# Optimization experiments

Hardware: AMD Instinct MI355X
Metric: run time of the kernel (lower is better)

Reference implementation:

```python
import jax, jax.numpy as jnp
import numpy as np

EPS = 1e-12

def _l2norm(x):
    # F.normalize(p=2, dim=1) with eps clamp on the norm
    n = jnp.linalg.norm(x, axis=1, keepdims=True)
    return x / jnp.maximum(n, EPS)

def _xavier_uniform(key, shape, gain=1.414):
    fan_in, fan_out = shape[-1], shape[0]
    a = gain * np.sqrt(6.0 / (fan_in + fan_out))
    return jax.random.uniform(key, shape, jnp.float32, -a, a)

def setup_inputs() -> dict:
    NUM_ENT, NUM_REL, D, E, B = 100000, 500, 512, 150000, 4096
    key = jax.random.key(0)
    ks = jax.random.split(key, 12)
    heads = jax.random.randint(ks[0], (B, 1), 0, NUM_ENT)
    rels  = jax.random.randint(ks[1], (B, 1), 0, NUM_REL)
    tails = jax.random.randint(ks[2], (B, 1), 0, NUM_ENT)
    triples = jnp.concatenate([heads, rels, tails], axis=1)           # [B,3]
    node_list = jax.random.randint(ks[3], (2, E), 0, NUM_ENT)          # [2,E] (src,dst)
    edge_list = jax.random.randint(ks[4], (E,), 0, NUM_REL)            # [E] relation per edge
    return {
        "triples": triples,
        "node_list": node_list,
        "edge_list": edge_list,
        "ent_emb_init": jax.random.normal(ks[5], (NUM_ENT, D), jnp.float32),
        "rel_emb_init": jax.random.normal(ks[6], (NUM_REL, D), jnp.float32),
        "W_1": _xavier_uniform(ks[7], (D, D)),
        "W_a": _xavier_uniform(ks[8], (1, D)),
        "g_0": _xavier_uniform(ks[9], (1, D)),
        "W_E": _xavier_uniform(ks[10], (D, D)),
        "W_R": _xavier_uniform(ks[11], (D, D)),
    }

def reference(triples, node_list, edge_list, ent_emb_init, rel_emb_init,
              W_1, W_a, g_0, W_E, W_R):
    num_ent = ent_emb_init.shape[0]
    e0 = _l2norm(ent_emb_init)                      # normalized entity table [N,D]
    src, dst = node_list[0], node_list[1]
    h_i = e0[src]                                   # [E,D]
    h_j = e0[dst]                                   # [E,D]
    g_k = rel_emb_init[edge_list]                   # [E,D]

    # c_ijk = W_1 @ (h_j*g_k)^T  -> kept edge-major as [E,D]
    c = (h_j * g_k) @ W_1.T                         # [E,D]
    a = -jax.nn.leaky_relu((h_i * jnp.tanh(c)) @ W_a[0], 0.2)   # [E]
    c_base = (h_i * g_0) @ W_1.T                    # [E,D]
    a_base = -jax.nn.leaky_relu((h_i * jnp.tanh(c_base)) @ W_a[0], 0.2)  # [E]

    a_exp = jnp.exp(a)                              # [E]
    ab_exp = jnp.exp(a_base)                        # [E]

    # segment-softmax denominator: sum of edge exps per source node + baseline term
    a_exp_sum = jax.ops.segment_sum(a_exp[:, None], src, num_segments=num_ent)  # [N,1]
    # baseline exp depends only on src node -> duplicate scatter-set writes identical values
    ab_sorted = jnp.zeros_like(a_exp_sum).at[src].set(ab_exp[:, None])           # [N,1]
    denom = ab_sorted + a_exp_sum
    denom = jnp.where(denom == 0.0, EPS, denom)

    # weighted scatter-aggregate of messages (dropout omitted: eval-mode identity)
    ac = a_exp[:, None] * c                         # [E,D]
    ac_base = ab_exp[:, None] * c_base              # [E,D]
    a_new = jax.ops.segment_sum(ac, src, num_segments=num_ent)                   # [N,D]
    ab_new = jnp.zeros_like(a_new).at[src].set(ac_base)                          # [N,D]

    h_prime = jax.nn.elu((ab_new + a_new) / denom)  # [N,D]
    ent_new = _l2norm(e0 @ W_E + h_prime)           # [N,D]
    rel_new = rel_emb_init @ W_R                    # [R,D]

    head = ent_new[triples[:, 0]][:, None, :]       # [B,1,D]
    rel  = rel_new[triples[:, 1]][:, None, :]       # [B,1,D]
    tail = ent_new[triples[:, 2]][:, None, :]       # [B,1,D]
    return jnp.concatenate([head, rel, tail], axis=1)  # [B,3,D]
```

## Files before the change

kernel.cpp:

```cpp
#include <hip/hip_runtime.h>
#include <cmath>


#define DDIM 512
#define MAXM 65536
#define GBM 128
#define GBN 128

typedef __attribute__((ext_vector_type(8))) short short8;
typedef __attribute__((ext_vector_type(4))) short short4v;
typedef __attribute__((ext_vector_type(4))) float fv4;
typedef unsigned short u16;

__device__ __forceinline__ float elu1(float x) { return x > 0.f ? x : expm1f(x); }
__device__ __forceinline__ float sexp(float x) {
    float lr = x >= 0.f ? x : 0.2f * x;
    return expf(-lr);
}
__device__ __forceinline__ u16 f2bf(float x) {
    unsigned u = __float_as_uint(x);
    u += 0x7FFFu + ((u >> 16) & 1u);
    return (u16)(u >> 16);
}
__device__ __forceinline__ float bf2f(u16 h) {
    return __uint_as_float((unsigned)h << 16);
}
__device__ __forceinline__ void cvt8(const float* v, short8& h8, short8& l8) {
    #pragma unroll
    for (int i = 0; i < 8; i++) {
        u16 h = f2bf(v[i]);
        h8[i] = (short)h;
        l8[i] = (short)f2bf(v[i] - bf2f(h));
    }
}
__device__ __forceinline__ void gld16(const void* g, void* l) {
    __builtin_amdgcn_global_load_lds(
        (const __attribute__((address_space(1))) unsigned int*)g,
        (__attribute__((address_space(3))) unsigned int*)l,
        16, 0, 0);
}

__global__ __launch_bounds__(128)
void invnorm_sel_kernel(const float* __restrict__ emb, const int* __restrict__ slotNode,
                        const int* __restrict__ rowsL, const int* __restrict__ dstIdx,
                        const int* __restrict__ Mdev, int NS, float* __restrict__ invN)
{
    __shared__ float ws2[2];
    int total = NS + min(MAXM, *Mdev);
    int t = threadIdx.x;
    for (int q = blockIdx.x; q < total; q += gridDim.x) {
        int n = (q < NS) ? slotNode[q] : dstIdx[rowsL[q - NS]];
        float4 v = *(const float4*)(emb + (size_t)n * DDIM + t * 4);
        float s = v.x*v.x + v.y*v.y + v.z*v.z + v.w*v.w;
        #pragma unroll
        for (int off = 32; off > 0; off >>= 1) s += __shfl_down(s, off);
        if ((t & 63) == 0) ws2[t >> 6] = s;
        __syncthreads();
        if (t == 0) invN[n] = 1.f / fmaxf(sqrtf(ws2[0] + ws2[1]), 1e-12f);
        __syncthreads();
    }
}

__global__ __launch_bounds__(128)
void l2norm_kernel(float* __restrict__ data)
{
    int r = blockIdx.x, t = threadIdx.x;
    size_t o = (size_t)r * DDIM + t * 4;
    float4 v = *(const float4*)(data + o);
    float s = v.x*v.x + v.y*v.y + v.z*v.z + v.w*v.w;
    #pragma unroll
    for (int off = 32; off > 0; off >>= 1) s += __shfl_down(s, off);
    __shared__ float ws2[2];
    if ((t & 63) == 0) ws2[t >> 6] = s;
    __syncthreads();
    float inv = 1.f / fmaxf(sqrtf(ws2[0] + ws2[1]), 1e-12f);
    *(float4*)(data + o) = make_float4(v.x*inv, v.y*inv, v.z*inv, v.w*inv);
}

__global__ void hist_kernel(const int* __restrict__ src, int* __restrict__ cnt, int E)
{
    int e = blockIdx.x * 256 + threadIdx.x;
    if (e < E) atomicAdd(&cnt[src[e]], 1);
}

__global__ __launch_bounds__(1024)
void scan1_kernel(const int* __restrict__ in, int* __restrict__ out,
                  int* __restrict__ blockTot, int n)
{
    __shared__ int sh[1024];
    int t = threadIdx.x;
    int i = blockIdx.x * 1024 + t;
    int v = (i < n) ? in[i] : 0;
    sh[t] = v;
    __syncthreads();
    for (int off = 1; off < 1024; off <<= 1) {
        int x = (t >= off) ? sh[t - off] : 0;
        __syncthreads();
        sh[t] += x;
        __syncthreads();
    }
    if (i < n) out[i] = sh[t] - v;
    if (t == 1023) blockTot[blockIdx.x] = sh[1023];
}

__global__ __launch_bounds__(1024)
void scan2_kernel(const int* __restrict__ blockTot, int* __restrict__ blockOff,
                  int* __restrict__ outLast, int G)
{
    __shared__ int sh[1024];
    int t = threadIdx.x;
    int v = (t < G) ? blockTot[t] : 0;
    sh[t] = v;
    __syncthreads();
    for (int off = 1; off < 1024; off <<= 1) {
        int x = (t >= off) ? sh[t - off] : 0;
        __syncthreads();
        sh[t] += x;
        __syncthreads();
    }
    if (t < G) blockOff[t] = sh[t] - v;
    if (t == 1023) *outLast = sh[1023];
}

__global__ __launch_bounds__(1024)
void scan3_dual_kernel(int* __restrict__ out, const int* __restrict__ blockOff,
                       int* __restrict__ out2, int n)
{
    int i = blockIdx.x * 1024 + threadIdx.x;
    if (i < n) {
        int v = out[i] + blockOff[blockIdx.x];
        out[i] = v;
        if (out2) out2[i] = v;
    }
}

__global__ void bucket_slotdeg_kernel(const int* __restrict__ src, int* __restrict__ cursor,
                                      int* __restrict__ edge_ids, int E,
                                      const int* __restrict__ triples, const int* __restrict__ rowSt,
                                      int* __restrict__ slotNode, int* __restrict__ deg, int NS)
{
    int i = blockIdx.x * 256 + threadIdx.x;
    if (i < E) { int p = atomicAdd(&cursor[src[i]], 1); edge_ids[p] = i; }
    int r = i - E;
    if (r >= 0 && r < NS) {
        int b = r >> 1, p = (r & 1) * 2;
        int n = triples[b * 3 + p];
        slotNode[r] = n;
        deg[r] = rowSt[n + 1] - rowSt[n];
    }
}

__global__ void fill_rows_kernel(const int* __restrict__ slotNode, const int* __restrict__ rowSt,
                                 const int* __restrict__ edgeIds, const int* __restrict__ slotOff,
                                 int* __restrict__ rows, int* __restrict__ srcL, int NS)
{
    int r = blockIdx.x * 256 + threadIdx.x;
    if (r >= NS) return;
    int n = slotNode[r];
    int gs = rowSt[n], d = rowSt[n + 1] - gs, mo = slotOff[r];
    for (int j = 0; j < d && mo + j < MAXM; j++) {
        rows[mo + j] = edgeIds[gs + j];
        srcL[mo + j] = n;
    }
}


__global__ __launch_bounds__(256)
void wfrag_kernel(const float* __restrict__ W1, const float* __restrict__ WE,
                  const float* __restrict__ WR, const float* __restrict__ relEmb,
                  int R,
                  u16* __restrict__ W1H, u16* __restrict__ W1L,
                  u16* __restrict__ WEH, u16* __restrict__ WEL,
                  u16* __restrict__ WRH, u16* __restrict__ WRL,
                  u16* __restrict__ ArH, u16* __restrict__ ArL)
{
    int mat = blockIdx.y;
    const float* src = (mat == 0) ? W1 : (mat == 1) ? WE : (mat == 2) ? WR : relEmb;
    u16* hi = (mat == 0) ? W1H : (mat == 1) ? WEH : (mat == 2) ? WRH : ArH;
    u16* lo = (mat == 0) ? W1L : (mat == 1) ? WEL : (mat == 2) ? WRL : ArL;
    bool tr = (mat == 1 || mat == 2);
    int rows = (mat == 3) ? R : DDIM;

    int nt = ((rows + 127) >> 7) << 3;
    int wid = threadIdx.x >> 6, lane = threadIdx.x & 63;
    int l15 = lane & 15, seg = (lane >> 4) * 8;
    for (int rt = blockIdx.x * 4 + wid; rt < nt; rt += gridDim.x * 4) {
        int r = min(rt * 16 + l15, rows - 1);
        size_t base = (size_t)rt * 8192 + (size_t)lane * 8;
        #pragma unroll 2
        for (int kt = 0; kt < 16; kt++) {
            float v[8];
            if (!tr) {
                const float* p = src + (size_t)r * DDIM + seg + kt * 32;
                float4 x0 = *(const float4*)p;
                float4 x1 = *(const float4*)(p + 4);
                v[0]=x0.x; v[1]=x0.y; v[2]=x0.z; v[3]=x0.w;
                v[4]=x1.x; v[5]=x1.y; v[6]=x1.z; v[7]=x1.w;
            } else {
                int k0 = kt * 32 + seg;
                #pragma unroll
                for (int i = 0; i < 8; i++)
                    v[i] = src[(size_t)(k0 + i) * DDIM + r];
            }
            short8 h8, l8; cvt8(v, h8, l8);
            *(short8*)(hi + base + (size_t)kt * 512) = h8;
            *(short8*)(lo + base + (size_t)kt * 512) = l8;
        }
    }
}

__global__ __launch_bounds__(256)
void afrag_es_kernel(const float* __restrict__ entEmb, const float* __restrict__ invN,
                     const float* __restrict__ relEmb, const float* __restrict__ g0,
                     const int* __restrict__ rowsL, const int* __restrict__ dstIdx,
                     const int* __restrict__ relIdx, const int* __restrict__ slotNode,
                     const int* __restrict__ Mdev, int NS,
                     u16* __restrict__ AeH, u16* __restrict__ AeL,
                     u16* __restrict__ As1H, u16* __restrict__ As1L,
                     u16* __restrict__ As3H, u16* __restrict__ As3L)
{
    int M = min(MAXM, *Mdev);
    int ntE = ((M + 127) >> 7) << 3;
    int ntS = ((NS + 127) >> 7) << 3;
    int total = ntE + ntS;
    int wid = threadIdx.x >> 6, lane = threadIdx.x & 63;
    int l15 = lane & 15, seg = (lane >> 4) * 8;

    for (int g = blockIdx.x * 4 + wid; g < total; g += gridDim.x * 4) {
        if (g < ntE) {
            int rt = g;
            int m = min(rt * 16 + l15, M - 1);
            int e = rowsL[m];
            int dn = dstIdx[e], rl = relIdx[e];
            float sc = invN[dn];
            const float* ep = entEmb + (size_t)dn * DDIM + seg;
            const float* rp = relEmb + (size_t)rl * DDIM + seg;
            size_t base = (size_t)rt * 8192 + (size_t)lane * 8;
            #pragma unroll 4
            for (int kt = 0; kt < 16; kt++) {
                float4 x0 = *(const float4*)(ep + kt * 32);
                float4 x1 = *(const float4*)(ep + kt * 32 + 4);
                float4 y0 = *(const float4*)(rp + kt * 32);
                float4 y1 = *(const float4*)(rp + kt * 32 + 4);
                float v[8] = {sc*x0.x*y0.x, sc*x0.y*y0.y, sc*x0.z*y0.z, sc*x0.w*y0.w,
                              sc*x1.x*y1.x, sc*x1.y*y1.y, sc*x1.z*y1.z, sc*x1.w*y1.w};
                short8 h8, l8; cvt8(v, h8, l8);
                *(short8*)(AeH + base + (size_t)kt * 512) = h8;
                *(short8*)(AeL + base + (size_t)kt * 512) = l8;
            }
        } else {
            int rt = g - ntE;
            int r = min(rt * 16 + l15, NS - 1);
            int n = slotNode[r];
            float sc = invN[n];
            const float* ep = entEmb + (size_t)n * DDIM + seg;
            const float* gp = g0 + seg;
            size_t base = (size_t)rt * 8192 + (size_t)lane * 8;
            #pragma unroll 2
            for (int kt = 0; kt < 16; kt++) {
                float4 x0 = *(const float4*)(ep + kt * 32);
                float4 x1 = *(const float4*)(ep + kt * 32 + 4);
                float4 y0 = *(const float4*)(gp + kt * 32);
                float4 y1 = *(const float4*)(gp + kt * 32 + 4);
                float v3[8] = {sc*x0.x, sc*x0.y, sc*x0.z, sc*x0.w,
                               sc*x1.x, sc*x1.y, sc*x1.z, sc*x1.w};
                float v1[8] = {v3[0]*y0.x, v3[1]*y0.y, v3[2]*y0.z, v3[3]*y0.w,
                               v3[4]*y1.x, v3[5]*y1.y, v3[6]*y1.z, v3[7]*y1.w};
                short8 h8, l8;
                cvt8(v3, h8, l8);
                *(short8*)(As3H + base + (size_t)kt * 512) = h8;
                *(short8*)(As3L + base + (size_t)kt * 512) = l8;
                cvt8(v1, h8, l8);
                *(short8*)(As1H + base + (size_t)kt * 512) = h8;
                *(short8*)(As1L + base + (size_t)kt * 512) = l8;
            }
        }
    }
}

template<int EPI, bool DEVM>
__global__ __launch_bounds__(256)
void gemm_frag_k(const u16* __restrict__ Ahi, const u16* __restrict__ Alo,
                 const u16* __restrict__ Bhi, const u16* __restrict__ Blo,
                 const u16* __restrict__ A2hi, const u16* __restrict__ A2lo,
                 const u16* __restrict__ B2hi, const u16* __restrict__ B2lo,
                 const float* __restrict__ entEmb, const float* __restrict__ invNorm,
                 const int* __restrict__ srcMap, const float* __restrict__ Wa,
                 float* __restrict__ scoreOut, const float* __restrict__ invDenom,
                 float* __restrict__ Cout,
                 int Mhost, const int* __restrict__ Mdev)
{
    __shared__ __align__(1024) u16 lds[2][32 * 512];

    int M = DEVM ? min(MAXM, *Mdev) : Mhost;
    int lane = threadIdx.x & 63, wid = threadIdx.x >> 6;
    int waveM = wid >> 1, waveN = wid & 1;
    int quad = lane >> 4, l15 = lane & 15;
    int n0 = blockIdx.y * GBN;

    const u16* g1 = (wid == 0) ? Ahi : (wid == 1) ? Alo : (wid == 2) ? Bhi : Blo;
    const u16* g2 = (EPI == 4)
        ? ((wid == 0) ? A2hi : (wid == 1) ? A2lo : (wid == 2) ? B2hi : B2lo)
        : nullptr;
    int ldsChunk0 = wid * 8;
    const int NKK = (EPI == 4) ? 32 : 16;

    for (int mt = blockIdx.x; mt * GBM < M; mt += gridDim.x) {
        int m0 = mt * GBM;
        int rowBase = (wid < 2) ? (m0 >> 4) : (n0 >> 4);
        const u16* s1 = g1 + (size_t)rowBase * 8192 + (size_t)lane * 8;
        const u16* s2 = (EPI == 4) ? g2 + (size_t)rowBase * 8192 + (size_t)lane * 8 : nullptr;

        fv4 acc[4][4];
        #pragma unroll
        for (int i = 0; i < 4; i++)
            #pragma unroll
            for (int j = 0; j < 4; j++) acc[i][j] = fv4{0.f, 0.f, 0.f, 0.f};

        int cur = 0;
        #pragma unroll
        for (int q = 0; q < 8; q++)
            gld16(s1 + (size_t)q * 8192, &lds[0][(ldsChunk0 + q) * 512]);
        __syncthreads();

        for (int kk = 0; kk < NKK; kk++) {
            int kn = kk + 1;
            if (kn < NKK) {
                const u16* sp = (EPI == 4 && kn >= 16) ? s2 : s1;
                size_t go = (size_t)(kn & 15) * 512;
                #pragma unroll
                for (int q = 0; q < 8; q++)
                    gld16(sp + (size_t)q * 8192 + go,
                          &lds[cur ^ 1][(ldsChunk0 + q) * 512]);
            }
            const u16* buf = &lds[cur][0];
            short8 aH[4], aL[4], bH[4], bL[4];
            #pragma unroll
            for (int i = 0; i < 4; i++) {
                aH[i] = *(const short8*)&buf[(waveM * 4 + i) * 512 + lane * 8];
                aL[i] = *(const short8*)&buf[(8 + waveM * 4 + i) * 512 + lane * 8];
                bH[i] = *(const short8*)&buf[(16 + waveN * 4 + i) * 512 + lane * 8];
                bL[i] = *(const short8*)&buf[(24 + waveN * 4 + i) * 512 + lane * 8];
            }
            #pragma unroll
            for (int i = 0; i < 4; i++)
                #pragma unroll
                for (int j = 0; j < 4; j++) {
                    acc[i][j] = __builtin_amdgcn_mfma_f32_16x16x32_bf16(aH[i], bH[j], acc[i][j], 0, 0, 0);
                    acc[i][j] = __builtin_amdgcn_mfma_f32_16x16x32_bf16(aH[i], bL[j], acc[i][j], 0, 0, 0);
                    acc[i][j] = __builtin_amdgcn_mfma_f32_16x16x32_bf16(aL[i], bH[j], acc[i][j], 0, 0, 0);
                }
            if (EPI == 4 && kk == 15) {
                #pragma unroll
                for (int i = 0; i < 4; i++)
                    #pragma unroll
                    for (int reg = 0; reg < 4; reg++) {
                        int gm = m0 + waveM * 64 + i * 16 + quad * 4 + reg;
                        float idv = invDenom[min(gm, M - 1)];
                        #pragma unroll
                        for (int j = 0; j < 4; j++)
                            acc[i][j][reg] = elu1(acc[i][j][reg] * idv);
                    }
            }
            __syncthreads();
            cur ^= 1;
        }

        if (EPI == 1) {
            #pragma unroll
            for (int i = 0; i < 4; i++) {
                #pragma unroll
                for (int reg = 0; reg < 4; reg++) {
                    int gm = m0 + waveM * 64 + i * 16 + quad * 4 + reg;
                    bool valid = gm < M;
                    int gmc = valid ? gm : 0;
                    int srcn = srcMap[gmc];
                    float invs = invNorm[srcn];
                    float s = 0.f;
                    #pragma unroll
                    for (int j = 0; j < 4; j++) {
                        int col = n0 + waveN * 64 + j * 16 + l15;
                        float hv = entEmb[(size_t)srcn * DDIM + col];
                        float wv = Wa[col];
                        s += tanhf(acc[i][j][reg]) * hv * wv;
                    }
                    s *= invs;
                    s += __shfl_xor(s, 8); s += __shfl_xor(s, 4);
                    s += __shfl_xor(s, 2); s += __shfl_xor(s, 1);
                    if (l15 == 0 && valid) atomicAdd(scoreOut + gm, s);
                }
            }
        } else {
            #pragma unroll
            for (int i = 0; i < 4; i++) {
                #pragma unroll
                for (int reg = 0; reg < 4; reg++) {
                    int gm = m0 + waveM * 64 + i * 16 + quad * 4 + reg;
                    if (gm >= M) continue;
                    #pragma unroll
                    for (int j = 0; j < 4; j++) {
                        int col = n0 + waveN * 64 + j * 16 + l15;
                        Cout[(size_t)gm * DDIM + col] = acc[i][j][reg];
                    }
                }
            }
        }
    }
}

__global__ __launch_bounds__(128)
void build_p_kernel(const float* __restrict__ entEmb, const float* __restrict__ invNorm,
                    const float* __restrict__ relEmb, const float* __restrict__ g0,
                    const int* __restrict__ slotNode, const int* __restrict__ rowSt,
                    const int* __restrict__ edgeIds, const int* __restrict__ dstIdx,
                    const int* __restrict__ relIdx, const int* __restrict__ slotOff,
                    const float* __restrict__ scoreE, const float* __restrict__ scoreS,
                    int NS,
                    u16* __restrict__ ApH, u16* __restrict__ ApL,
                    float* __restrict__ invDenom)
{
    int r = blockIdx.x, t = threadIdx.x;
    float4 acc = make_float4(0.f, 0.f, 0.f, 0.f);
    float dInv = 1.f;
    if (r < NS) {
        int n = slotNode[r];
        int gs = rowSt[n], d = rowSt[n + 1] - gs;
        if (d > 0) {
            int mo = slotOff[r];
            float ab = sexp(scoreS[r]);
            float sc = ab * invNorm[n];
            float4 ev = *(const float4*)(entEmb + (size_t)n * DDIM + t * 4);
            float4 gv = *(const float4*)(g0 + t * 4);
            acc = make_float4(sc*ev.x*gv.x, sc*ev.y*gv.y, sc*ev.z*gv.z, sc*ev.w*gv.w);
            float denom = ab;
            for (int j = 0; j < d; j++) {
                if (mo + j >= MAXM) break;
                int e = edgeIds[gs + j];
                float ae = sexp(scoreE[mo + j]);
                int dn = dstIdx[e], rl = relIdx[e];
                float s = ae * invNorm[dn];
                float4 dv = *(const float4*)(entEmb + (size_t)dn * DDIM + t * 4);
                float4 rv = *(const float4*)(relEmb + (size_t)rl * DDIM + t * 4);
                acc.x = fmaf(s, dv.x*rv.x, acc.x);
                acc.y = fmaf(s, dv.y*rv.y, acc.y);
                acc.z = fmaf(s, dv.z*rv.z, acc.z);
                acc.w = fmaf(s, dv.w*rv.w, acc.w);
                denom += ae;
            }
            dInv = 1.f / denom;
        }
    }
    int kt = t >> 3;
    int lane = (r & 15) + 16 * ((t >> 1) & 3);
    int j0 = (t & 1) * 4;
    size_t fo = (size_t)(r >> 4) * 8192 + (size_t)kt * 512 + (size_t)lane * 8 + j0;
    float v[4] = {acc.x, acc.y, acc.z, acc.w};
    short4v h4, l4;
    #pragma unroll
    for (int i = 0; i < 4; i++) {
        u16 h = f2bf(v[i]);
        h4[i] = (short)h;
        l4[i] = (short)f2bf(v[i] - bf2f(h));
    }
    *(short4v*)(ApH + fo) = h4;
    *(short4v*)(ApL + fo) = l4;
    if (t == 0 && r < NS) invDenom[r] = dInv;
}

__global__ __launch_bounds__(128)
void gather_out_kernel(const int* __restrict__ triples, const float* __restrict__ ENT,
                       const float* __restrict__ relnew, float* __restrict__ out)
{
    int r = blockIdx.x;
    int b = r / 3, j = r - b * 3;
    const float* srow;
    if (j == 1) srow = relnew + (size_t)triples[r] * DDIM;
    else        srow = ENT + (size_t)(b * 2 + (j == 2 ? 1 : 0)) * DDIM;
    int t = threadIdx.x * 4;
    *(float4*)(out + (size_t)r * DDIM + t) = *(const float4*)(srow + t);
}

extern "C" void kernel_launch(void* const* d_in, const int* in_sizes, int n_in,
                              void* d_out, int out_size, void* d_ws, size_t ws_size,
                              hipStream_t stream)
{
    const int*   triples = (const int*)  d_in[0];
    const int*   nodes   = (const int*)  d_in[1];
    const int*   edges   = (const int*)  d_in[2];
    const float* entEmb  = (const float*)d_in[3];
    const float* relEmb  = (const float*)d_in[4];
    const float* W1      = (const float*)d_in[5];
    const float* Wa      = (const float*)d_in[6];
    const float* g0      = (const float*)d_in[7];
    const float* WE      = (const float*)d_in[8];
    const float* WR      = (const float*)d_in[9];

    const int B  = in_sizes[0] / 3;
    const int E  = in_sizes[2];
    const int N  = in_sizes[3] / DDIM;
    const int R  = in_sizes[4] / DDIM;
    const int NS = 2 * B;
    const int* srcIdx = nodes;
    const int* dstIdx = nodes + E;

    char* ws = (char*)d_ws;
    size_t off = 0;
    auto carve = [&](size_t bytes) -> void* {
        void* p = ws + off;
        off = (off + bytes + 255) & ~(size_t)255;
        return p;
    };
    const int NS128 = ((NS + 127) / 128) * 128;
    const int R128  = ((R + 127) / 128) * 128;
    float* ENT      = (float*)carve((size_t)NS * DDIM * 4);
    float* relnew   = (float*)carve((size_t)R * DDIM * 4);
    float* invNorm  = (float*)carve((size_t)N * 4);
    float* scoreAll = (float*)carve((size_t)(MAXM + NS) * 4);
    float* score_e  = scoreAll;
    float* score_s  = scoreAll + MAXM;
    float* invDen   = (float*)carve((size_t)NS * 4);
    int*   cnt      = (int*)carve((size_t)N * 4);
    int*   rowSt    = (int*)carve((size_t)(N + 1) * 4);
    int*   cursor   = (int*)carve((size_t)N * 4);
    int*   edgeIds  = (int*)carve((size_t)E * 4);
    int*   slotNode = (int*)carve((size_t)NS * 4);
    int*   deg      = (int*)carve((size_t)NS * 4);
    int*   slotOff  = (int*)carve((size_t)(NS + 1) * 4);
    int*   rowsL    = (int*)carve((size_t)MAXM * 4);
    int*   srcL     = (int*)carve((size_t)MAXM * 4);
    int*   blockTot = (int*)carve((size_t)1024 * 4);
    int*   blockOff = (int*)carve((size_t)1024 * 4);
    u16* AeH  = (u16*)carve((size_t)MAXM * DDIM * 2);
    u16* AeL  = (u16*)carve((size_t)MAXM * DDIM * 2);
    u16* As1H = (u16*)carve((size_t)NS128 * DDIM * 2);
    u16* As1L = (u16*)carve((size_t)NS128 * DDIM * 2);
    u16* As3H = (u16*)carve((size_t)NS128 * DDIM * 2);
    u16* As3L = (u16*)carve((size_t)NS128 * DDIM * 2);
    u16* ApH  = (u16*)carve((size_t)NS128 * DDIM * 2);
    u16* ApL  = (u16*)carve((size_t)NS128 * DDIM * 2);
    u16* ArH  = (u16*)carve((size_t)R128 * DDIM * 2);
    u16* ArL  = (u16*)carve((size_t)R128 * DDIM * 2);
    u16* W1H  = (u16*)carve((size_t)DDIM * DDIM * 2);
    u16* W1L  = (u16*)carve((size_t)DDIM * DDIM * 2);
    u16* WEH  = (u16*)carve((size_t)DDIM * DDIM * 2);
    u16* WEL  = (u16*)carve((size_t)DDIM * DDIM * 2);
    u16* WRH  = (u16*)carve((size_t)DDIM * DDIM * 2);
    u16* WRL  = (u16*)carve((size_t)DDIM * DDIM * 2);
    (void)ws_size; (void)n_in; (void)out_size;

    hipMemsetAsync(cnt, 0, (size_t)N * 4, stream);
    hist_kernel<<<(E + 255) / 256, 256, 0, stream>>>(srcIdx, cnt, E);
    {
        int G = (N + 1023) / 1024;
        scan1_kernel<<<G, 1024, 0, stream>>>(cnt, rowSt, blockTot, N);
        scan2_kernel<<<1, 1024, 0, stream>>>(blockTot, blockOff, rowSt + N, G);
        scan3_dual_kernel<<<G, 1024, 0, stream>>>(rowSt, blockOff, cursor, N);
    }
    bucket_slotdeg_kernel<<<(E + NS + 255) / 256, 256, 0, stream>>>(
        srcIdx, cursor, edgeIds, E, triples, rowSt, slotNode, deg, NS);
    {
        int G = (NS + 1023) / 1024;
        scan1_kernel<<<G, 1024, 0, stream>>>(deg, slotOff, blockTot, NS);
        scan2_kernel<<<1, 1024, 0, stream>>>(blockTot, blockOff, slotOff + NS, G);
        scan3_dual_kernel<<<G, 1024, 0, stream>>>(slotOff, blockOff, nullptr, NS);
    }
    fill_rows_kernel<<<(NS + 255) / 256, 256, 0, stream>>>(slotNode, rowSt, edgeIds,
                                                           slotOff, rowsL, srcL, NS);
    const int* Mdev = slotOff + NS;

    invnorm_sel_kernel<<<4096, 128, 0, stream>>>(entEmb, slotNode, rowsL, dstIdx,
                                                 Mdev, NS, invNorm);

    wfrag_kernel<<<dim3(8, 4), 256, 0, stream>>>(W1, WE, WR, relEmb, R,
                                                 W1H, W1L, WEH, WEL, WRH, WRL, ArH, ArL);

    afrag_es_kernel<<<256, 256, 0, stream>>>(entEmb, invNorm, relEmb, g0,
                                             rowsL, dstIdx, edges, slotNode,
                                             Mdev, NS,
                                             AeH, AeL, As1H, As1L, As3H, As3L);

    hipMemsetAsync(scoreAll, 0, (size_t)(MAXM + NS) * 4, stream);
    dim3 gEdge(128, DDIM / GBN);
    gemm_frag_k<1, true><<<gEdge, 256, 0, stream>>>(
        AeH, AeL, W1H, W1L, nullptr, nullptr, nullptr, nullptr,
        entEmb, invNorm, srcL, Wa, score_e, nullptr, nullptr, 0, Mdev);
    dim3 gSlot((NS + GBM - 1) / GBM, DDIM / GBN);
    gemm_frag_k<1, false><<<gSlot, 256, 0, stream>>>(
        As1H, As1L, W1H, W1L, nullptr, nullptr, nullptr, nullptr,
        entEmb, invNorm, slotNode, Wa, score_s, nullptr, nullptr, NS, nullptr);

    build_p_kernel<<<NS128, 128, 0, stream>>>(entEmb, invNorm, relEmb, g0, slotNode,
                                              rowSt, edgeIds, dstIdx, edges, slotOff,
                                              score_e, score_s, NS, ApH, ApL, invDen);

    gemm_frag_k<4, false><<<gSlot, 256, 0, stream>>>(
        ApH, ApL, W1H, W1L, As3H, As3L, WEH, WEL,
        entEmb, invNorm, nullptr, nullptr, nullptr, invDen, ENT, NS, nullptr);
    l2norm_kernel<<<NS, 128, 0, stream>>>(ENT);

    dim3 gRel((R + GBM - 1) / GBM, DDIM / GBN);
    gemm_frag_k<0, false><<<gRel, 256, 0, stream>>>(
        ArH, ArL, WRH, WRL, nullptr, nullptr, nullptr, nullptr,
        entEmb, invNorm, nullptr, nullptr, nullptr, nullptr, relnew, R, nullptr);

    gather_out_kernel<<<B * 3, 128, 0, stream>>>(triples, ENT, relnew, (float*)d_out);
}
```

Baseline: 496.4 us.

## Fuse scans, inverse-norm, score GEMMs, tail GEMMs and final normalization to cut launches

```diff
diff --git a/kernel.cpp b/kernel.cpp
--- a/kernel.cpp
+++ b/kernel.cpp
@@ -11,6 +11,7 @@
 typedef __attribute__((ext_vector_type(4))) short short4v;
 typedef __attribute__((ext_vector_type(4))) float fv4;
 typedef unsigned short u16;
+typedef unsigned long long u64;
 
 __device__ __forceinline__ float elu1(float x) { return x > 0.f ? x : expm1f(x); }
 __device__ __forceinline__ float sexp(float x) {
@@ -40,43 +41,6 @@
         16, 0, 0);
 }
 
-__global__ __launch_bounds__(128)
-void invnorm_sel_kernel(const float* __restrict__ emb, const int* __restrict__ slotNode,
-                        const int* __restrict__ rowsL, const int* __restrict__ dstIdx,
-                        const int* __restrict__ Mdev, int NS, float* __restrict__ invN)
-{
-    __shared__ float ws2[2];
-    int total = NS + min(MAXM, *Mdev);
-    int t = threadIdx.x;
-    for (int q = blockIdx.x; q < total; q += gridDim.x) {
-        int n = (q < NS) ? slotNode[q] : dstIdx[rowsL[q - NS]];
-        float4 v = *(const float4*)(emb + (size_t)n * DDIM + t * 4);
-        float s = v.x*v.x + v.y*v.y + v.z*v.z + v.w*v.w;
-        #pragma unroll
-        for (int off = 32; off > 0; off >>= 1) s += __shfl_down(s, off);
-        if ((t & 63) == 0) ws2[t >> 6] = s;
-        __syncthreads();
-        if (t == 0) invN[n] = 1.f / fmaxf(sqrtf(ws2[0] + ws2[1]), 1e-12f);
-        __syncthreads();
-    }
-}
-
-__global__ __launch_bounds__(128)
-void l2norm_kernel(float* __restrict__ data)
-{
-    int r = blockIdx.x, t = threadIdx.x;
-    size_t o = (size_t)r * DDIM + t * 4;
-    float4 v = *(const float4*)(data + o);
-    float s = v.x*v.x + v.y*v.y + v.z*v.z + v.w*v.w;
-    #pragma unroll
-    for (int off = 32; off > 0; off >>= 1) s += __shfl_down(s, off);
-    __shared__ float ws2[2];
-    if ((t & 63) == 0) ws2[t >> 6] = s;
-    __syncthreads();
-    float inv = 1.f / fmaxf(sqrtf(ws2[0] + ws2[1]), 1e-12f);
-    *(float4*)(data + o) = make_float4(v.x*inv, v.y*inv, v.z*inv, v.w*inv);
-}
-
 __global__ void hist_kernel(const int* __restrict__ src, int* __restrict__ cnt, int E)
 {
     int e = blockIdx.x * 256 + threadIdx.x;
@@ -84,54 +48,85 @@
 }
 
 __global__ __launch_bounds__(1024)
-void scan1_kernel(const int* __restrict__ in, int* __restrict__ out,
-                  int* __restrict__ blockTot, int n)
+void scan_lookback_kernel(const int* __restrict__ in, int* __restrict__ out,
+                          int* __restrict__ out2, int n,
+                          int* __restrict__ ticket, u64* __restrict__ state)
 {
     __shared__ int sh[1024];
+    __shared__ int bidSh, exSh;
     int t = threadIdx.x;
-    int i = blockIdx.x * 1024 + t;
+    if (t == 0) bidSh = atomicAdd(ticket, 1);
+    __syncthreads();
+    int bid = bidSh;
+    int i = bid * 1024 + t;
     int v = (i < n) ? in[i] : 0;
     sh[t] = v;
     __syncthreads();
-    for (int off = 1; off < 1024; off <<= 1) {
-        int x = (t >= off) ? sh[t - off] : 0;
+    for (int o = 1; o < 1024; o <<= 1) {
+        int x = (t >= o) ? sh[t - o] : 0;
         __syncthreads();
         sh[t] += x;
         __syncthreads();
     }
-    if (i < n) out[i] = sh[t] - v;
-    if (t == 1023) blockTot[blockIdx.x] = sh[1023];
+    int incl = sh[t];
+    int agg = sh[1023];
+    if (t == 0) {
+        u64 pub = (bid == 0) ? ((2ull << 32) | (unsigned)agg)
+                             : ((1ull << 32) | (unsigned)agg);
+        __hip_atomic_store(&state[bid], pub, __ATOMIC_RELEASE, __HIP_MEMORY_SCOPE_AGENT);
+        int ex = 0;
+        if (bid > 0) {
+            int p = bid - 1;
+            for (;;) {
+                u64 s;
+                do {
+                    s = __hip_atomic_load(&state[p], __ATOMIC_ACQUIRE, __HIP_MEMORY_SCOPE_AGENT);
+                } while ((s >> 32) == 0);
+                ex += (int)(unsigned)s;
+                if ((s >> 32) == 2ull) break;
+                p--;
+            }
+            __hip_atomic_store(&state[bid], (2ull << 32) | (unsigned)(ex + agg),
+                               __ATOMIC_RELEASE, __HIP_MEMORY_SCOPE_AGENT);
+        }
+        exSh = ex;
+    }
+    __syncthreads();
+    int ex = exSh;
+    if (i < n) {
+        int e = ex + incl - v;
+        out[i] = e;
+        if (out2) out2[i] = e;
+        if (i == n - 1) out[n] = ex + incl;
+    }
 }
 
 __global__ __launch_bounds__(1024)
-void scan2_kernel(const int* __restrict__ blockTot, int* __restrict__ blockOff,
-                  int* __restrict__ outLast, int G)
+void scan_small_kernel(const int* __restrict__ in, int* __restrict__ out, int n)
 {
     __shared__ int sh[1024];
+    __shared__ int carrySh;
     int t = threadIdx.x;
-    int v = (t < G) ? blockTot[t] : 0;
-    sh[t] = v;
+    if (t == 0) carrySh = 0;
     __syncthreads();
-    for (int off = 1; off < 1024; off <<= 1) {
-        int x = (t >= off) ? sh[t - off] : 0;
+    for (int base = 0; base < n; base += 1024) {
+        int i = base + t;
+        int v = (i < n) ? in[i] : 0;
+        sh[t] = v;
         __syncthreads();
-        sh[t] += x;
+        for (int o = 1; o < 1024; o <<= 1) {
+            int x = (t >= o) ? sh[t - o] : 0;
+            __syncthreads();
+            sh[t] += x;
+            __syncthreads();
+        }
+        int carry = carrySh;
+        if (i < n) out[i] = carry + sh[t] - v;
         __syncthreads();
-    }
-    if (t < G) blockOff[t] = sh[t] - v;
-    if (t == 1023) *outLast = sh[1023];
-}
-
-__global__ __launch_bounds__(1024)
-void scan3_dual_kernel(int* __restrict__ out, const int* __restrict__ blockOff,
-                       int* __restrict__ out2, int n)
-{
-    int i = blockIdx.x * 1024 + threadIdx.x;
-    if (i < n) {
-        int v = out[i] + blockOff[blockIdx.x];
-        out[i] = v;
-        if (out2) out2[i] = v;
-    }
+        if (t == 1023) carrySh = carry + sh[1023];
+        __syncthreads();
+    }
+    if (t == 0) out[n] = carrySh;
 }
 
 __global__ void bucket_slotdeg_kernel(const int* __restrict__ src, int* __restrict__ cursor,
@@ -210,7 +205,7 @@
 }
 
 __global__ __launch_bounds__(256)
-void afrag_es_kernel(const float* __restrict__ entEmb, const float* __restrict__ invN,
+void afrag_es_kernel(const float* __restrict__ entEmb, float* __restrict__ invN,
                      const float* __restrict__ relEmb, const float* __restrict__ g0,
                      const int* __restrict__ rowsL, const int* __restrict__ dstIdx,
                      const int* __restrict__ relIdx, const int* __restrict__ slotNode,
@@ -219,7 +214,7 @@
                      u16* __restrict__ As1H, u16* __restrict__ As1L,
                      u16* __restrict__ As3H, u16* __restrict__ As3L)
 {
-    int M = min(MAXM, *Mdev);
+    int M = max(1, min(MAXM, *Mdev));
     int ntE = ((M + 127) >> 7) << 3;
     int ntS = ((NS + 127) >> 7) << 3;
     int total = ntE + ntS;
@@ -227,15 +222,31 @@
     int l15 = lane & 15, seg = (lane >> 4) * 8;
 
     for (int g = blockIdx.x * 4 + wid; g < total; g += gridDim.x * 4) {
-        if (g < ntE) {
-            int rt = g;
+        bool isE = g < ntE;
+        int rt = isE ? g : g - ntE;
+        int node, rl = 0;
+        if (isE) {
             int m = min(rt * 16 + l15, M - 1);
             int e = rowsL[m];
-            int dn = dstIdx[e], rl = relIdx[e];
-            float sc = invN[dn];
-            const float* ep = entEmb + (size_t)dn * DDIM + seg;
+            node = dstIdx[e]; rl = relIdx[e];
+        } else {
+            node = slotNode[min(rt * 16 + l15, NS - 1)];
+        }
+        const float* ep = entEmb + (size_t)node * DDIM + seg;
+        float ss = 0.f;
+        for (int kt = 0; kt < 16; kt++) {
+            float4 x0 = *(const float4*)(ep + kt * 32);
+            float4 x1 = *(const float4*)(ep + kt * 32 + 4);
+            ss += x0.x*x0.x + x0.y*x0.y + x0.z*x0.z + x0.w*x0.w
+                + x1.x*x1.x + x1.y*x1.y + x1.z*x1.z + x1.w*x1.w;
+        }
+        ss += __shfl_xor(ss, 16);
+        ss += __shfl_xor(ss, 32);
+        float sc = 1.f / fmaxf(sqrtf(ss), 1e-12f);
+        if (lane < 16) invN[node] = sc;
+        size_t base = (size_t)rt * 8192 + (size_t)lane * 8;
+        if (isE) {
             const float* rp = relEmb + (size_t)rl * DDIM + seg;
-            size_t base = (size_t)rt * 8192 + (size_t)lane * 8;
             #pragma unroll 4
             for (int kt = 0; kt < 16; kt++) {
                 float4 x0 = *(const float4*)(ep + kt * 32);
@@ -249,13 +260,7 @@
                 *(short8*)(AeL + base + (size_t)kt * 512) = l8;
             }
         } else {
-            int rt = g - ntE;
-            int r = min(rt * 16 + l15, NS - 1);
-            int n = slotNode[r];
-            float sc = invN[n];
-            const float* ep = entEmb + (size_t)n * DDIM + seg;
             const float* gp = g0 + seg;
-            size_t base = (size_t)rt * 8192 + (size_t)lane * 8;
             #pragma unroll 2
             for (int kt = 0; kt < 16; kt++) {
                 float4 x0 = *(const float4*)(ep + kt * 32);
@@ -278,38 +283,34 @@
     }
 }
 
-template<int EPI, bool DEVM>
 __global__ __launch_bounds__(256)
-void gemm_frag_k(const u16* __restrict__ Ahi, const u16* __restrict__ Alo,
-                 const u16* __restrict__ Bhi, const u16* __restrict__ Blo,
-                 const u16* __restrict__ A2hi, const u16* __restrict__ A2lo,
-                 const u16* __restrict__ B2hi, const u16* __restrict__ B2lo,
-                 const float* __restrict__ entEmb, const float* __restrict__ invNorm,
-                 const int* __restrict__ srcMap, const float* __restrict__ Wa,
-                 float* __restrict__ scoreOut, const float* __restrict__ invDenom,
-                 float* __restrict__ Cout,
-                 int Mhost, const int* __restrict__ Mdev)
+void gemm_score_k(const u16* __restrict__ AeH, const u16* __restrict__ AeL,
+                  const u16* __restrict__ As1H, const u16* __restrict__ As1L,
+                  const u16* __restrict__ W1H, const u16* __restrict__ W1L,
+                  const float* __restrict__ entEmb, const float* __restrict__ invNorm,
+                  const int* __restrict__ srcL, const int* __restrict__ slotNode,
+                  const float* __restrict__ Wa, float* __restrict__ scoreP,
+                  const int* __restrict__ Mdev, int NS, int SCLEN)
 {
     __shared__ __align__(1024) u16 lds[2][32 * 512];
-
-    int M = DEVM ? min(MAXM, *Mdev) : Mhost;
+    int M = max(1, min(MAXM, *Mdev));
+    int TE = (M + 127) >> 7, TS = (NS + 127) >> 7;
+    int total = TE + TS;
     int lane = threadIdx.x & 63, wid = threadIdx.x >> 6;
     int waveM = wid >> 1, waveN = wid & 1;
     int quad = lane >> 4, l15 = lane & 15;
     int n0 = blockIdx.y * GBN;
-
-    const u16* g1 = (wid == 0) ? Ahi : (wid == 1) ? Alo : (wid == 2) ? Bhi : Blo;
-    const u16* g2 = (EPI == 4)
-        ? ((wid == 0) ? A2hi : (wid == 1) ? A2lo : (wid == 2) ? B2hi : B2lo)
-        : nullptr;
     int ldsChunk0 = wid * 8;
-    const int NKK = (EPI == 4) ? 32 : 16;
-
-    for (int mt = blockIdx.x; mt * GBM < M; mt += gridDim.x) {
-        int m0 = mt * GBM;
+
+    for (int tt = blockIdx.x; tt < total; tt += gridDim.x) {
+        bool isE = tt < TE;
+        int m0 = (isE ? tt : tt - TE) * GBM;
+        int Mt = isE ? M : NS;
+        const u16* g1 = isE
+            ? ((wid == 0) ? AeH : (wid == 1) ? AeL : (wid == 2) ? W1H : W1L)
+            : ((wid == 0) ? As1H : (wid == 1) ? As1L : (wid == 2) ? W1H : W1L);
         int rowBase = (wid < 2) ? (m0 >> 4) : (n0 >> 4);
         const u16* s1 = g1 + (size_t)rowBase * 8192 + (size_t)lane * 8;
-        const u16* s2 = (EPI == 4) ? g2 + (size_t)rowBase * 8192 + (size_t)lane * 8 : nullptr;
 
         fv4 acc[4][4];
         #pragma unroll
@@ -323,14 +324,12 @@
             gld16(s1 + (size_t)q * 8192, &lds[0][(ldsChunk0 + q) * 512]);
         __syncthreads();
 
-        for (int kk = 0; kk < NKK; kk++) {
-            int kn = kk + 1;
-            if (kn < NKK) {
-                const u16* sp = (EPI == 4 && kn >= 16) ? s2 : s1;
-                size_t go = (size_t)(kn & 15) * 512;
+        for (int kk = 0; kk < 16; kk++) {
+            if (kk < 15) {
+                size_t go = (size_t)(kk + 1) * 512;
                 #pragma unroll
                 for (int q = 0; q < 8; q++)
-                    gld16(sp + (size_t)q * 8192 + go,
+                    gld16(s1 + (size_t)q * 8192 + go,
                           &lds[cur ^ 1][(ldsChunk0 + q) * 512]);
             }
             const u16* buf = &lds[cur][0];
@@ -350,13 +349,119 @@
                     acc[i][j] = __builtin_amdgcn_mfma_f32_16x16x32_bf16(aH[i], bL[j], acc[i][j], 0, 0, 0);
                     acc[i][j] = __builtin_amdgcn_mfma_f32_16x16x32_bf16(aL[i], bH[j], acc[i][j], 0, 0, 0);
                 }
-            if (EPI == 4 && kk == 15) {
+            __syncthreads();
+            cur ^= 1;
+        }
+
+        int base = isE ? 0 : MAXM;
+        #pragma unroll
+        for (int i = 0; i < 4; i++) {
+            #pragma unroll
+            for (int reg = 0; reg < 4; reg++) {
+                int gm = m0 + waveM * 64 + i * 16 + quad * 4 + reg;
+                bool valid = gm < Mt;
+                int gmc = valid ? gm : 0;
+                int srcn = isE ? srcL[gmc] : slotNode[gmc];
+                float invs = invNorm[srcn];
+                float s = 0.f;
+                #pragma unroll
+                for (int j = 0; j < 4; j++) {
+                    int col = n0 + waveN * 64 + j * 16 + l15;
+                    float hv = entEmb[(size_t)srcn * DDIM + col];
+                    float wv = Wa[col];
+                    s += tanhf(acc[i][j][reg]) * hv * wv;
+                }
+                s *= invs;
+                s += __shfl_xor(s, 8); s += __shfl_xor(s, 4);
+                s += __shfl_xor(s, 2); s += __shfl_xor(s, 1);
+                if (l15 == 0 && valid)
+                    scoreP[(size_t)blockIdx.y * SCLEN + base + gm] = s;
+            }
+        }
+    }
+}
+
+__global__ __launch_bounds__(256)
+void gemm_tail_k(const u16* __restrict__ ApH, const u16* __restrict__ ApL,
+                 const u16* __restrict__ W1H, const u16* __restrict__ W1L,
+                 const u16* __restrict__ As3H, const u16* __restrict__ As3L,
+                 const u16* __restrict__ WEH, const u16* __restrict__ WEL,
+                 const u16* __restrict__ ArH, const u16* __restrict__ ArL,
+                 const u16* __restrict__ WRH, const u16* __restrict__ WRL,
+                 const float* __restrict__ invDenom,
+                 float* __restrict__ ENT, float* __restrict__ relnew, int NS, int R)
+{
+    __shared__ __align__(1024) u16 lds[2][32 * 512];
+    int lane = threadIdx.x & 63, wid = threadIdx.x >> 6;
+    int waveM = wid >> 1, waveN = wid & 1;
+    int quad = lane >> 4, l15 = lane & 15;
+    int n0 = blockIdx.y * GBN;
+    int TS = (NS + 127) >> 7, TR = (R + 127) >> 7;
+    int total = TS + TR;
+    int ldsChunk0 = wid * 8;
+
+    for (int tt = blockIdx.x; tt < total; tt += gridDim.x) {
+        bool fused = tt < TS;
+        int m0 = (fused ? tt : tt - TS) * GBM;
+        int Mt = fused ? NS : R;
+        float* Cout = fused ? ENT : relnew;
+        const u16* g1 = fused
+            ? ((wid == 0) ? ApH : (wid == 1) ? ApL : (wid == 2) ? W1H : W1L)
+            : ((wid == 0) ? ArH : (wid == 1) ? ArL : (wid == 2) ? WRH : WRL);
+        const u16* g2 = fused
+            ? ((wid == 0) ? As3H : (wid == 1) ? As3L : (wid == 2) ? WEH : WEL)
+            : nullptr;
+        int nkk = fused ? 32 : 16;
+        int rowBase = (wid < 2) ? (m0 >> 4) : (n0 >> 4);
+        const u16* s1 = g1 + (size_t)rowBase * 8192 + (size_t)lane * 8;
+        const u16* s2 = fused ? g2 + (size_t)rowBase * 8192 + (size_t)lane * 8 : nullptr;
+
+        fv4 acc[4][4];
+        #pragma unroll
+        for (int i = 0; i < 4; i++)
+            #pragma unroll
+            for (int j = 0; j < 4; j++) acc[i][j] = fv4{0.f, 0.f, 0.f, 0.f};
+
+        int cur = 0;
+        #pragma unroll
+        for (int q = 0; q < 8; q++)
+            gld16(s1 + (size_t)q * 8192, &lds[0][(ldsChunk0 + q) * 512]);
+        __syncthreads();
+
+        for (int kk = 0; kk < nkk; kk++) {
+            int kn = kk + 1;
+            if (kn < nkk) {
+                const u16* sp = (fused && kn >= 16) ? s2 : s1;
+                size_t go = (size_t)(kn & 15) * 512;
+                #pragma unroll
+                for (int q = 0; q < 8; q++)
+                    gld16(sp + (size_t)q * 8192 + go,
+                          &lds[cur ^ 1][(ldsChunk0 + q) * 512]);
+            }
+            const u16* buf = &lds[cur][0];
+            short8 aH[4], aL[4], bH[4], bL[4];
+            #pragma unroll
+            for (int i = 0; i < 4; i++) {
+                aH[i] = *(const short8*)&buf[(waveM * 4 + i) * 512 + lane * 8];
+                aL[i] = *(const short8*)&buf[(8 + waveM * 4 + i) * 512 + lane * 8];
+                bH[i] = *(const short8*)&buf[(16 + waveN * 4 + i) * 512 + lane * 8];
+                bL[i] = *(const short8*)&buf[(24 + waveN * 4 + i) * 512 + lane * 8];
+            }
+            #pragma unroll
+            for (int i = 0; i < 4; i++)
+                #pragma unroll
+                for (int j = 0; j < 4; j++) {
+                    acc[i][j] = __builtin_amdgcn_mfma_f32_16x16x32_bf16(aH[i], bH[j], acc[i][j], 0, 0, 0);
+                    acc[i][j] = __builtin_amdgcn_mfma_f32_16x16x32_bf16(aH[i], bL[j], acc[i][j], 0, 0, 0);
+                    acc[i][j] = __builtin_amdgcn_mfma_f32_16x16x32_bf16(aL[i], bH[j], acc[i][j], 0, 0, 0);
+                }
+            if (fused && kk == 15) {
                 #pragma unroll
                 for (int i = 0; i < 4; i++)
                     #pragma unroll
                     for (int reg = 0; reg < 4; reg++) {
                         int gm = m0 + waveM * 64 + i * 16 + quad * 4 + reg;
-                        float idv = invDenom[min(gm, M - 1)];
+                        float idv = invDenom[min(gm, Mt - 1)];
                         #pragma unroll
                         for (int j = 0; j < 4; j++)
                             acc[i][j][reg] = elu1(acc[i][j][reg] * idv);
@@ -366,42 +471,16 @@
             cur ^= 1;
         }
 
-        if (EPI == 1) {
-            #pragma unroll
-            for (int i = 0; i < 4; i++) {
-                #pragma unroll
-                for (int reg = 0; reg < 4; reg++) {
-                    int gm = m0 + waveM * 64 + i * 16 + quad * 4 + reg;
-                    bool valid = gm < M;
-                    int gmc = valid ? gm : 0;
-                    int srcn = srcMap[gmc];
-                    float invs = invNorm[srcn];
-                    float s = 0.f;
-                    #pragma unroll
-                    for (int j = 0; j < 4; j++) {
-                        int col = n0 + waveN * 64 + j * 16 + l15;
-                        float hv = entEmb[(size_t)srcn * DDIM + col];
-                        float wv = Wa[col];
-                        s += tanhf(acc[i][j][reg]) * hv * wv;
-                    }
-                    s *= invs;
-                    s += __shfl_xor(s, 8); s += __shfl_xor(s, 4);
-                    s += __shfl_xor(s, 2); s += __shfl_xor(s, 1);
-                    if (l15 == 0 && valid) atomicAdd(scoreOut + gm, s);
-                }
-            }
-        } else {
-            #pragma unroll
-            for (int i = 0; i < 4; i++) {
-                #pragma unroll
-                for (int reg = 0; reg < 4; reg++) {
-                    int gm = m0 + waveM * 64 + i * 16 + quad * 4 + reg;
-                    if (gm >= M) continue;
-                    #pragma unroll
-                    for (int j = 0; j < 4; j++) {
-                        int col = n0 + waveN * 64 + j * 16 + l15;
-                        Cout[(size_t)gm * DDIM + col] = acc[i][j][reg];
-                    }
+        #pragma unroll
+        for (int i = 0; i < 4; i++) {
+            #pragma unroll
+            for (int reg = 0; reg < 4; reg++) {
+                int gm = m0 + waveM * 64 + i * 16 + quad * 4 + reg;
+                if (gm >= Mt) continue;
+                #pragma unroll
+                for (int j = 0; j < 4; j++) {
+                    int col = n0 + waveN * 64 + j * 16 + l15;
+                    Cout[(size_t)gm * DDIM + col] = acc[i][j][reg];
                 }
             }
         }
@@ -414,8 +493,7 @@
                     const int* __restrict__ slotNode, const int* __restrict__ rowSt,
                     const int* __restrict__ edgeIds, const int* __restrict__ dstIdx,
                     const int* __restrict__ relIdx, const int* __restrict__ slotOff,
-                    const float* __restrict__ scoreE, const float* __restrict__ scoreS,
-                    int NS,
+                    const float* __restrict__ scoreP, int SCLEN, int NS,
                     u16* __restrict__ ApH, u16* __restrict__ ApL,
                     float* __restrict__ invDenom)
 {
@@ -427,7 +505,9 @@
         int gs = rowSt[n], d = rowSt[n + 1] - gs;
         if (d > 0) {
             int mo = slotOff[r];
-            float ab = sexp(scoreS[r]);
+            int si = MAXM + r;
+            float ab = sexp(scoreP[si] + scoreP[SCLEN + si]
+                          + scoreP[2 * SCLEN + si] + scoreP[3 * SCLEN + si]);
             float sc = ab * invNorm[n];
             float4 ev = *(const float4*)(entEmb + (size_t)n * DDIM + t * 4);
             float4 gv = *(const float4*)(g0 + t * 4);
@@ -436,7 +516,9 @@
             for (int j = 0; j < d; j++) {
                 if (mo + j >= MAXM) break;
                 int e = edgeIds[gs + j];
-                float ae = sexp(scoreE[mo + j]);
+                int ei = mo + j;
+                float ae = sexp(scoreP[ei] + scoreP[SCLEN + ei]
+                              + scoreP[2 * SCLEN + ei] + scoreP[3 * SCLEN + ei]);
                 int dn = dstIdx[e], rl = relIdx[e];
                 float s = ae * invNorm[dn];
                 float4 dv = *(const float4*)(entEmb + (size_t)dn * DDIM + t * 4);
@@ -473,11 +555,23 @@
 {
     int r = blockIdx.x;
     int b = r / 3, j = r - b * 3;
-    const float* srow;
-    if (j == 1) srow = relnew + (size_t)triples[r] * DDIM;
-    else        srow = ENT + (size_t)(b * 2 + (j == 2 ? 1 : 0)) * DDIM;
-    int t = threadIdx.x * 4;
-    *(float4*)(out + (size_t)r * DDIM + t) = *(const float4*)(srow + t);
+    int t = threadIdx.x;
+    size_t oo = (size_t)r * DDIM + t * 4;
+    if (j == 1) {
+        const float* srow = relnew + (size_t)triples[r] * DDIM;
+        *(float4*)(out + oo) = *(const float4*)(srow + t * 4);
+        return;
+    }
+    const float* srow = ENT + (size_t)(b * 2 + (j == 2 ? 1 : 0)) * DDIM;
+    float4 v = *(const float4*)(srow + t * 4);
+    float s = v.x*v.x + v.y*v.y + v.z*v.z + v.w*v.w;
+    #pragma unroll
+    for (int off = 32; off > 0; off >>= 1) s += __shfl_down(s, off);
+    __shared__ float ws2[2];
+    if ((t & 63) == 0) ws2[t >> 6] = s;
+    __syncthreads();
+    float inv = 1.f / fmaxf(sqrtf(ws2[0] + ws2[1]), 1e-12f);
+    *(float4*)(out + oo) = make_float4(v.x*inv, v.y*inv, v.z*inv, v.w*inv);
 }
 
 extern "C" void kernel_launch(void* const* d_in, const int* in_sizes, int n_in,
@@ -512,14 +606,17 @@
     };
     const int NS128 = ((NS + 127) / 128) * 128;
     const int R128  = ((R + 127) / 128) * 128;
+    const int SCLEN = MAXM + NS128;
     float* ENT      = (float*)carve((size_t)NS * DDIM * 4);
     float* relnew   = (float*)carve((size_t)R * DDIM * 4);
     float* invNorm  = (float*)carve((size_t)N * 4);
-    float* scoreAll = (float*)carve((size_t)(MAXM + NS) * 4);
-    float* score_e  = scoreAll;
-    float* score_s  = scoreAll + MAXM;
+    float* scoreP   = (float*)carve((size_t)4 * SCLEN * 4);
     float* invDen   = (float*)carve((size_t)NS * 4);
+    char*  zbase    = ws + off;
     int*   cnt      = (int*)carve((size_t)N * 4);
+    int*   ticket   = (int*)carve(256);
+    u64*   stateN   = (u64*)carve((size_t)1024 * 8);
+    size_t zbytes   = (size_t)((ws + off) - zbase);
     int*   rowSt    = (int*)carve((size_t)(N + 1) * 4);
     int*   cursor   = (int*)carve((size_t)N * 4);
     int*   edgeIds  = (int*)carve((size_t)E * 4);
@@ -528,8 +625,6 @@
     int*   slotOff  = (int*)carve((size_t)(NS + 1) * 4);
     int*   rowsL    = (int*)carve((size_t)MAXM * 4);
     int*   srcL     = (int*)carve((size_t)MAXM * 4);
-    int*   blockTot = (int*)carve((size_t)1024 * 4);
-    int*   blockOff = (int*)carve((size_t)1024 * 4);
     u16* AeH  = (u16*)carve((size_t)MAXM * DDIM * 2);
     u16* AeL  = (u16*)carve((size_t)MAXM * DDIM * 2);
     u16* As1H = (u16*)carve((size_t)NS128 * DDIM * 2);
@@ -548,60 +643,31 @@
     u16* WRL  = (u16*)carve((size_t)DDIM * DDIM * 2);
     (void)ws_size; (void)n_in; (void)out_size;
 
-    hipMemsetAsync(cnt, 0, (size_t)N * 4, stream);
+    hipMemsetAsync(zbase, 0, zbytes, stream);
     hist_kernel<<<(E + 255) / 256, 256, 0, stream>>>(srcIdx, cnt, E);
-    {
-        int G = (N + 1023) / 1024;
-        scan1_kernel<<<G, 1024, 0, stream>>>(cnt, rowSt, blockTot, N);
-        scan2_kernel<<<1, 1024, 0, stream>>>(blockTot, blockOff, rowSt + N, G);
-        scan3_dual_kernel<<<G, 1024, 0, stream>>>(rowSt, blockOff, cursor, N);
-    }
+    scan_lookback_kernel<<<(N + 1023) / 1024, 1024, 0, stream>>>(
+        cnt, rowSt, cursor, N, ticket, stateN);
     bucket_slotdeg_kernel<<<(E + NS + 255) / 256, 256, 0, stream>>>(
         srcIdx, cursor, edgeIds, E, triples, rowSt, slotNode, deg, NS);
-    {
-        int G = (NS + 1023) / 1024;
-        scan1_kernel<<<G, 1024, 0, stream>>>(deg, slotOff, blockTot, NS);
-        scan2_kernel<<<1, 1024, 0, stream>>>(blockTot, blockOff, slotOff + NS, G);
-        scan3_dual_kernel<<<G, 1024, 0, stream>>>(slotOff, blockOff, nullptr, NS);
-    }
+    scan_small_kernel<<<1, 1024, 0, stream>>>(deg, slotOff, NS);
+    const int* Mdev = slotOff + NS;
     fill_rows_kernel<<<(NS + 255) / 256, 256, 0, stream>>>(slotNode, rowSt, edgeIds,
                                                            slotOff, rowsL, srcL, NS);
-    const int* Mdev = slotOff + NS;
-
-    invnorm_sel_kernel<<<4096, 128, 0, stream>>>(entEmb, slotNode, rowsL, dstIdx,
-                                                 Mdev, NS, invNorm);
-
     wfrag_kernel<<<dim3(8, 4), 256, 0, stream>>>(W1, WE, WR, relEmb, R,
                                                  W1H, W1L, WEH, WEL, WRH, WRL, ArH, ArL);
-
     afrag_es_kernel<<<256, 256, 0, stream>>>(entEmb, invNorm, relEmb, g0,
                                              rowsL, dstIdx, edges, slotNode,
                                              Mdev, NS,
                                              AeH, AeL, As1H, As1L, As3H, As3L);
-
-    hipMemsetAsync(scoreAll, 0, (size_t)(MAXM + NS) * 4, stream);
-    dim3 gEdge(128, DDIM / GBN);
-    gemm_frag_k<1, true><<<gEdge, 256, 0, stream>>>(
-        AeH, AeL, W1H, W1L, nullptr, nullptr, nullptr, nullptr,
-        entEmb, invNorm, srcL, Wa, score_e, nullptr, nullptr, 0, Mdev);
-    dim3 gSlot((NS + GBM - 1) / GBM, DDIM / GBN);
-    gemm_frag_k<1, false><<<gSlot, 256, 0, stream>>>(
-        As1H, As1L, W1H, W1L, nullptr, nullptr, nullptr, nullptr,
-        entEmb, invNorm, slotNode, Wa, score_s, nullptr, nullptr, NS, nullptr);
-
+    gemm_score_k<<<dim3(192, DDIM / GBN), 256, 0, stream>>>(
+        AeH, AeL, As1H, As1L, W1H, W1L, entEmb, invNorm, srcL, slotNode,
+        Wa, scoreP, Mdev, NS, SCLEN);
     build_p_kernel<<<NS128, 128, 0, stream>>>(entEmb, invNorm, relEmb, g0, slotNode,
                                               rowSt, edgeIds, dstIdx, edges, slotOff,
-                                              score_e, score_s, NS, ApH, ApL, invDen);
-
-    gemm_frag_k<4, false><<<gSlot, 256, 0, stream>>>(
-        ApH, ApL, W1H, W1L, As3H, As3L, WEH, WEL,
-        entEmb, invNorm, nullptr, nullptr, nullptr, invDen, ENT, NS, nullptr);
-    l2norm_kernel<<<NS, 128, 0, stream>>>(ENT);
-
-    dim3 gRel((R + GBM - 1) / GBM, DDIM / GBN);
-    gemm_frag_k<0, false><<<gRel, 256, 0, stream>>>(
-        ArH, ArL, WRH, WRL, nullptr, nullptr, nullptr, nullptr,
-        entEmb, invNorm, nullptr, nullptr, nullptr, nullptr, relnew, R, nullptr);
-
+                                              scoreP, SCLEN, NS, ApH, ApL, invDen);
+    int gTail = ((NS + GBM - 1) / GBM) + ((R + GBM - 1) / GBM);
+    gemm_tail_k<<<dim3(gTail, DDIM / GBN), 256, 0, stream>>>(
+        ApH, ApL, W1H, W1L, As3H, As3L, WEH, WEL, ArH, ArL, WRH, WRL,
+        invDen, ENT, relnew, NS, R);
     gather_out_kernel<<<B * 3, 128, 0, stream>>>(triples, ENT, relnew, (float*)d_out);
 }
```

Result: no change. 500.5 us (+0.8%).
